# Optimization experiments

Hardware: AMD Instinct MI355X
Metric: run time of the kernel (lower is better)

## Reference

```python
import jax, jax.numpy as jnp
import numpy as np

K = 7  # g_decode_kernel_size


def _linear(x, W, b):
    # torch nn.Linear: y = x @ W.T + b, W: [out, in]
    return jnp.matmul(x, W.T) + b


def _shifted_conv(x, w, b):
    # x: [B, D, L]; causal conv: pad left K-1 (== pad both sides K-1 then trim right K-1)
    y = jax.lax.conv_general_dilated(
        x, w, window_strides=(1,), padding=[(K - 1, 0)],
        dimension_numbers=("NCH", "OIH", "NCH"))
    y = y + b[None, :, None]  # [B, 2D, L]
    D = x.shape[1]
    gated = y[:, :D, :] * jax.nn.sigmoid(y[:, D:, :])
    return gated + x


def setup_inputs() -> dict:
    key = jax.random.key(0)
    ks = jax.random.split(key, 16)
    B, T, L = 64, 64, 32
    E_enc, emb, D, A, V = 1024, 512, 512, 512, 30000

    def rn(k, shape, fan_in):
        return jax.random.normal(k, shape, dtype=jnp.float32) * (1.0 / np.sqrt(fan_in))

    return {
        "features": jax.random.normal(ks[0], (B, T, E_enc), dtype=jnp.float32),
        "captions": jax.random.randint(ks[1], (B, L), 0, V),
        "lengths": jax.random.randint(ks[2], (B,), 0, L),
        "embed_W": jax.random.normal(ks[3], (V, emb), dtype=jnp.float32) * 0.02,
        "W1": rn(ks[4], (D, emb + E_enc), emb + E_enc),
        "b1": jnp.zeros((D,), jnp.float32),
        "conv_w1": rn(ks[5], (2 * D, D, K), D * K),
        "conv_b1": jnp.zeros((2 * D,), jnp.float32),
        "conv_w2": rn(ks[6], (2 * D, D, K), D * K),
        "conv_b2": jnp.zeros((2 * D,), jnp.float32),
        "Wenc": rn(ks[7], (A, E_enc), E_enc),
        "benc": jnp.zeros((A,), jnp.float32),
        "Wdec": rn(ks[8], (A, D), D),
        "bdec": jnp.zeros((A,), jnp.float32),
        "Wp": rn(ks[9], (1, A), A),
        "bp": jnp.zeros((1,), jnp.float32),
        "W2": rn(ks[10], (V, E_enc + D), E_enc + D),
        "b2": jnp.zeros((V,), jnp.float32),
    }


def reference(features, captions, lengths, embed_W, W1, b1, conv_w1, conv_b1,
              conv_w2, conv_b2, Wenc, benc, Wdec, bdec, Wp, bp, W2, b2):
    # features: [B, T, E_enc]; captions: [B, L] int
    embeddings = embed_W[captions]                      # [B, L, emb]
    enc_mean = jnp.mean(features, axis=1, keepdims=True)  # [B, 1, E_enc]
    enc_mean = jnp.broadcast_to(enc_mean, (features.shape[0], embeddings.shape[1], features.shape[2]))
    x = jnp.concatenate([enc_mean, embeddings], axis=2)  # [B, L, E_enc+emb]
    x = _linear(x, W1, b1)                               # [B, L, D]
    x = jnp.transpose(x, (0, 2, 1))                      # [B, D, L]
    x = _shifted_conv(x, conv_w1, conv_b1)
    x = _shifted_conv(x, conv_w2, conv_b2)
    decode = jnp.transpose(x, (0, 2, 1))[:, :-1, :]      # [B, L-1, D]

    # Attention (vectorized over decode steps). NOTE: original code computes
    # tanh but discards it (assigns to misspelled 'featrues'), so NO tanh here.
    f_att = _linear(features, Wenc, benc)                # [B, T, A]
    d_att = _linear(decode, Wdec, bdec)                  # [B, S, A]
    # linear_prob applied to (f_att[:,None,t]+d_att[:,s,None]) -> scalar scores
    scores = (f_att[:, None, :, :] + d_att[:, :, None, :]) @ Wp[0] + bp[0]  # [B, S, T]
    attw = jax.nn.softmax(scores, axis=-1)               # softmax over T
    ctx = jnp.einsum("bst,bte->bse", attw, features)     # [B, S, E_enc]

    out = jnp.concatenate([ctx, decode], axis=2)         # [B, S, E_enc+D]
    logits = _linear(out, W2, b2)                        # [B, S, vocab]
    return logits
```

## Files before the change

kernel.cpp:

```cpp
#include <hip/hip_runtime.h>
#include <hip/hip_bf16.h>
#include <math.h>

#define B 64
#define T 64
#define E_ENC 1024
#define EMB 512
#define D 512
#define L 32
#define S 31
#define A 512
#define V 30000
#define KSZ 7
#define KC (D * KSZ)

typedef __attribute__((ext_vector_type(8))) short bf16x8;
typedef __attribute__((ext_vector_type(4))) float f32x4;

__device__ __forceinline__ unsigned short f2bf(float f) {
  union { float f; unsigned int u; } x; x.f = f;
  unsigned int r = (x.u + 0x7fffu + ((x.u >> 16) & 1u)) >> 16;
  return (unsigned short)r;
}

__device__ __forceinline__ void gload_lds16(const void* g, void* l) {
  __builtin_amdgcn_global_load_lds(
      (const __attribute__((address_space(1))) unsigned int*)g,
      (__attribute__((address_space(3))) unsigned int*)l, 16, 0, 0);
}

__global__ void k_wv(const float* __restrict__ Wenc, const float* __restrict__ Wp,
                     const float* __restrict__ benc, float* __restrict__ wv,
                     float* __restrict__ c0) {
  __shared__ float sp[4][64];
  __shared__ float red[256];
  int el = threadIdx.x & 63, part = threadIdx.x >> 6;
  int e = blockIdx.x * 64 + el;
  float s = 0.f;
  for (int a = part * 128; a < part * 128 + 128; ++a)
    s += Wp[a] * Wenc[(size_t)a * E_ENC + e];
  sp[part][el] = s;
  __syncthreads();
  if (part == 0) wv[e] = sp[0][el] + sp[1][el] + sp[2][el] + sp[3][el];
  if (blockIdx.x == 0) {
    int t = threadIdx.x;
    float v = Wp[t] * benc[t] + Wp[t + 256] * benc[t + 256];
    red[t] = v;
    __syncthreads();
    for (int off = 128; off > 0; off >>= 1) {
      if (t < off) red[t] += red[t + off];
      __syncthreads();
    }
    if (t == 0) c0[0] = red[0];
  }
}

__global__ void k_mean_ctx(const float* __restrict__ features, const float* __restrict__ wv,
                           const float* __restrict__ c0, unsigned short* __restrict__ enc_meanb,
                           unsigned short* __restrict__ ctxb) {
  int b = blockIdx.x, tid = threadIdx.x;
  const float* fb = features + (size_t)b * T * E_ENC;
  __shared__ float s_attw[T];

  float m0 = 0, m1 = 0, m2 = 0, m3 = 0;
  for (int t = 0; t < T; ++t) {
    const float* r = fb + t * E_ENC;
    m0 += r[tid]; m1 += r[tid + 256]; m2 += r[tid + 512]; m3 += r[tid + 768];
  }
  size_t eb = (size_t)b * E_ENC;
  enc_meanb[eb + tid]       = f2bf(m0 * (1.f / 64.f));
  enc_meanb[eb + tid + 256] = f2bf(m1 * (1.f / 64.f));
  enc_meanb[eb + tid + 512] = f2bf(m2 * (1.f / 64.f));
  enc_meanb[eb + tid + 768] = f2bf(m3 * (1.f / 64.f));

  {
    int t = tid >> 2, part = tid & 3;
    const float* r = fb + t * E_ENC + part * 256;
    const float* wp = wv + part * 256;
    float s = 0.f;
    for (int e = 0; e < 256; e += 4) {
      float4 f4 = *(const float4*)(r + e);
      float4 w4 = *(const float4*)(wp + e);
      s += f4.x * w4.x + f4.y * w4.y + f4.z * w4.z + f4.w * w4.w;
    }
    s += __shfl_xor(s, 1);
    s += __shfl_xor(s, 2);
    if (part == 0) s_attw[t] = s + c0[0];
  }
  __syncthreads();
  if (tid < 64) {
    float v = s_attw[tid];
    float mx = v;
    #pragma unroll
    for (int off = 32; off > 0; off >>= 1) mx = fmaxf(mx, __shfl_xor(mx, off));
    float e = expf(v - mx);
    float sm = e;
    #pragma unroll
    for (int off = 32; off > 0; off >>= 1) sm += __shfl_xor(sm, off);
    s_attw[tid] = e / sm;
  }
  __syncthreads();
  float ca = 0, cb = 0, cc = 0, cd = 0;
  for (int t = 0; t < T; ++t) {
    float w = s_attw[t];
    const float* r = fb + t * E_ENC;
    ca += w * r[tid]; cb += w * r[tid + 256]; cc += w * r[tid + 512]; cd += w * r[tid + 768];
  }
  ctxb[eb + tid]       = f2bf(ca);
  ctxb[eb + tid + 256] = f2bf(cb);
  ctxb[eb + tid + 512] = f2bf(cc);
  ctxb[eb + tid + 768] = f2bf(cd);
}

__global__ void k_gather_emb(const float* __restrict__ embed_W,
                             const int* __restrict__ captions,
                             unsigned short* __restrict__ Xe) {
  int g = blockIdx.x, tid = threadIdx.x;
  int cap = captions[g];
  const float* src = embed_W + (size_t)cap * EMB;
  float2 v = *(const float2*)(src + tid * 2);
  unsigned int pk = (unsigned int)f2bf(v.x) | ((unsigned int)f2bf(v.y) << 16);
  *(unsigned int*)(Xe + (size_t)g * EMB + tid * 2) = pk;
}

__global__ void k_cvt_w1(const float* __restrict__ W1, unsigned short* __restrict__ w1b) {
  int d = blockIdx.x, tid = threadIdx.x;
  #pragma unroll
  for (int i = 0; i < 3; ++i) {
    int c = tid * 2 + i * 512;
    float2 v = *(const float2*)(W1 + (size_t)d * (E_ENC + EMB) + c);
    unsigned int pk = (unsigned int)f2bf(v.x) | ((unsigned int)f2bf(v.y) << 16);
    *(unsigned int*)(w1b + (size_t)d * (E_ENC + EMB) + c) = pk;
  }
}

__global__ __launch_bounds__(256) void k_x1f_mfma(
    const unsigned short* __restrict__ enc_meanb,
    const unsigned short* __restrict__ Xe,
    const unsigned short* __restrict__ w1b,
    const float* __restrict__ b1, float* __restrict__ x1) {
  __shared__ __align__(16) unsigned short As[64 * 64];
  __shared__ __align__(16) unsigned short Bs[64 * 64];
  int c0 = blockIdx.x * 64, g0 = blockIdx.y * 64;
  int tid = threadIdx.x, lane = tid & 63, wave = tid >> 6;
  int wr = wave >> 1, wc = wave & 1;
  int rsel = lane & 15, hi = lane >> 4;

  f32x4 acc[2][2];
  #pragma unroll
  for (int m = 0; m < 2; ++m)
    #pragma unroll
    for (int n = 0; n < 2; ++n) acc[m][n] = (f32x4){0.f, 0.f, 0.f, 0.f};

  int r1 = tid >> 3, s1 = tid & 7;
  int sw = (s1 ^ (r1 & 7)) * 8;
  const unsigned short* emA1 = enc_meanb + (size_t)(g0 >> 5) * 1024 + sw;
  const unsigned short* emA2 = enc_meanb + (size_t)((g0 >> 5) + 1) * 1024 + sw;
  const unsigned short* xeA1 = Xe + (size_t)(g0 + r1) * 512 + sw;
  const unsigned short* xeA2 = Xe + (size_t)(g0 + r1 + 32) * 512 + sw;
  const unsigned short* gB1 = w1b + (size_t)(c0 + r1) * (E_ENC + EMB) + sw;
  const unsigned short* gB2 = w1b + (size_t)(c0 + r1 + 32) * (E_ENC + EMB) + sw;
  unsigned short* aD1 = As + wave * 512;
  unsigned short* aD2 = As + 2048 + wave * 512;
  unsigned short* bD1 = Bs + wave * 512;
  unsigned short* bD2 = Bs + 2048 + wave * 512;

  int slot0 = hi ^ (rsel & 7);
  int slot1 = (4 + hi) ^ (rsel & 7);

  for (int kt = 0; kt < 24; ++kt) {
    const unsigned short *pA1, *pA2;
    if (kt < 16) { pA1 = emA1 + kt * 64; pA2 = emA2 + kt * 64; }
    else         { pA1 = xeA1 + (kt - 16) * 64; pA2 = xeA2 + (kt - 16) * 64; }
    gload_lds16(pA1, aD1);
    gload_lds16(pA2, aD2);
    gload_lds16(gB1, bD1);
    gload_lds16(gB2, bD2);
    gB1 += 64; gB2 += 64;
    __syncthreads();

    bf16x8 af[2][2], bfr[2][2];
    #pragma unroll
    for (int m = 0; m < 2; ++m) {
      int rowA = (wr * 32 + m * 16 + rsel) * 64;
      af[m][0] = *(const bf16x8*)(As + rowA + slot0 * 8);
      af[m][1] = *(const bf16x8*)(As + rowA + slot1 * 8);
    }
    #pragma unroll
    for (int n = 0; n < 2; ++n) {
      int rowB = (wc * 32 + n * 16 + rsel) * 64;
      bfr[n][0] = *(const bf16x8*)(Bs + rowB + slot0 * 8);
      bfr[n][1] = *(const bf16x8*)(Bs + rowB + slot1 * 8);
    }
    #pragma unroll
    for (int m = 0; m < 2; ++m)
      #pragma unroll
      for (int n = 0; n < 2; ++n) {
        acc[m][n] = __builtin_amdgcn_mfma_f32_16x16x32_bf16(af[m][0], bfr[n][0], acc[m][n], 0, 0, 0);
        acc[m][n] = __builtin_amdgcn_mfma_f32_16x16x32_bf16(af[m][1], bfr[n][1], acc[m][n], 0, 0, 0);
      }
    __syncthreads();
  }

  float bvv[2];
  #pragma unroll
  for (int n = 0; n < 2; ++n) bvv[n] = b1[c0 + wc * 32 + n * 16 + rsel];
  #pragma unroll
  for (int m = 0; m < 2; ++m)
    #pragma unroll
    for (int i = 0; i < 4; ++i) {
      int g = g0 + wr * 32 + m * 16 + hi * 4 + i;
      float* xr = x1 + (size_t)g * D;
      #pragma unroll
      for (int n = 0; n < 2; ++n) {
        int c = c0 + wc * 32 + n * 16 + rsel;
        xr[c] = acc[m][n][i] + bvv[n];
      }
    }
}

__global__ void k_im2col(const float* __restrict__ x, unsigned short* __restrict__ Xc) {
  int g = blockIdx.x, tid = threadIdx.x;
  int b = g >> 5, l = g & 31;
  unsigned short* row = Xc + (size_t)g * KC;
  const float* xb = x + (size_t)b * L * D;
  int d = tid * 2;
  #pragma unroll
  for (int k = 0; k < KSZ; ++k) {
    int lp = l + k - 6;
    unsigned int pk = 0;
    if (lp >= 0) {
      float2 v = *(const float2*)(xb + (size_t)lp * D + d);
      pk = (unsigned int)f2bf(v.x) | ((unsigned int)f2bf(v.y) << 16);
    }
    *(unsigned int*)(row + k * 512 + d) = pk;
  }
}

__global__ void k_cvt_wconv(const float* __restrict__ w, unsigned short* __restrict__ wb) {
  __shared__ float row[KC];
  int c = blockIdx.x, tid = threadIdx.x;
  const float* wr = w + (size_t)c * KC;
  for (int i = tid; i < KC; i += 256) row[i] = wr[i];
  __syncthreads();
  unsigned short* ob = wb + (size_t)c * KC;
  int dp = tid * 2;
  #pragma unroll
  for (int k = 0; k < KSZ; ++k) {
    unsigned int pk = (unsigned int)f2bf(row[dp * 7 + k]) |
                      ((unsigned int)f2bf(row[(dp + 1) * 7 + k]) << 16);
    *(unsigned int*)(ob + k * 512 + dp) = pk;
  }
}

template <int OUT_BF16>
__global__ __launch_bounds__(256) void k_conv_glu(
    const unsigned short* __restrict__ Xc, const unsigned short* __restrict__ wb,
    const float* __restrict__ bias, const float* __restrict__ xres,
    float* __restrict__ outf, unsigned short* __restrict__ outh) {
  __shared__ __align__(16) unsigned char csmem[32768];
  unsigned short (*As)[64 * 64] = (unsigned short (*)[64 * 64])csmem;
  unsigned short (*Bs)[64 * 64] = (unsigned short (*)[64 * 64])(csmem + 16384);
  int c0 = blockIdx.x * 32, g0 = blockIdx.y * 64;
  int tid = threadIdx.x, lane = tid & 63, wave = tid >> 6;
  int wr = wave >> 1, wc = wave & 1;
  int rsel = lane & 15, hi = lane >> 4;

  f32x4 acc[2][2];
  #pragma unroll
  for (int m = 0; m < 2; ++m)
    #pragma unroll
    for (int n = 0; n < 2; ++n) acc[m][n] = (f32x4){0.f, 0.f, 0.f, 0.f};

  int r1 = tid >> 3, s1 = tid & 7;
  int sw = (s1 ^ (r1 & 7)) * 8;
  const unsigned short* gA1 = Xc + (size_t)(g0 + r1) * KC + sw;
  const unsigned short* gA2 = Xc + (size_t)(g0 + r1 + 32) * KC + sw;
  const unsigned short* gB1 = wb + (size_t)(c0 + r1) * KC + sw;
  const unsigned short* gB2 = wb + (size_t)(512 + c0 + r1) * KC + sw;

  int slot0 = hi ^ (rsel & 7);
  int slot1 = (4 + hi) ^ (rsel & 7);

  gload_lds16(gA1, &As[0][wave * 512]);
  gload_lds16(gA2, &As[0][2048 + wave * 512]);
  gload_lds16(gB1, &Bs[0][wave * 512]);
  gload_lds16(gB2, &Bs[0][2048 + wave * 512]);
  gA1 += 64; gA2 += 64; gB1 += 64; gB2 += 64;
  __syncthreads();

  int cur = 0;
  for (int kt = 0; kt < KC / 64; ++kt) {
    if (kt + 1 < KC / 64) {
      int nb = cur ^ 1;
      gload_lds16(gA1, &As[nb][wave * 512]);
      gload_lds16(gA2, &As[nb][2048 + wave * 512]);
      gload_lds16(gB1, &Bs[nb][wave * 512]);
      gload_lds16(gB2, &Bs[nb][2048 + wave * 512]);
      gA1 += 64; gA2 += 64; gB1 += 64; gB2 += 64;
    }

    bf16x8 af[2][2], bfr[2][2];
    #pragma unroll
    for (int m = 0; m < 2; ++m) {
      int rowA = (wr * 32 + m * 16 + rsel) * 64;
      af[m][0] = *(const bf16x8*)(&As[cur][rowA + slot0 * 8]);
      af[m][1] = *(const bf16x8*)(&As[cur][rowA + slot1 * 8]);
    }
    #pragma unroll
    for (int n = 0; n < 2; ++n) {
      int rowB = (wc * 32 + n * 16 + rsel) * 64;
      bfr[n][0] = *(const bf16x8*)(&Bs[cur][rowB + slot0 * 8]);
      bfr[n][1] = *(const bf16x8*)(&Bs[cur][rowB + slot1 * 8]);
    }
    #pragma unroll
    for (int m = 0; m < 2; ++m)
      #pragma unroll
      for (int n = 0; n < 2; ++n) {
        acc[m][n] = __builtin_amdgcn_mfma_f32_16x16x32_bf16(af[m][0], bfr[n][0], acc[m][n], 0, 0, 0);
        acc[m][n] = __builtin_amdgcn_mfma_f32_16x16x32_bf16(af[m][1], bfr[n][1], acc[m][n], 0, 0, 0);
      }
    __syncthreads();
    cur ^= 1;
  }

  float* sb = (float*)csmem;
  float bvv[2];
  #pragma unroll
  for (int n = 0; n < 2; ++n)
    bvv[n] = wc ? bias[512 + c0 + n * 16 + rsel] : bias[c0 + n * 16 + rsel];
  if (wc) {
    #pragma unroll
    for (int m = 0; m < 2; ++m)
      #pragma unroll
      for (int i = 0; i < 4; ++i) {
        int lr = wr * 32 + m * 16 + hi * 4 + i;
        #pragma unroll
        for (int n = 0; n < 2; ++n)
          sb[lr * 33 + n * 16 + rsel] = acc[m][n][i] + bvv[n];
      }
  }
  __syncthreads();
  if (!wc) {
    #pragma unroll
    for (int m = 0; m < 2; ++m)
      #pragma unroll
      for (int i = 0; i < 4; ++i) {
        int lr = wr * 32 + m * 16 + hi * 4 + i;
        int g = g0 + lr;
        const float* xr = xres + (size_t)g * 512 + c0;
        #pragma unroll
        for (int n = 0; n < 2; ++n) {
          int d = n * 16 + rsel;
          float ya = acc[m][n][i] + bvv[n];
          float yb = sb[lr * 33 + d];
          float val = ya / (1.f + expf(-yb)) + xr[d];
          if (OUT_BF16) outh[(size_t)g * 512 + c0 + d] = f2bf(val);
          else          outf[(size_t)g * 512 + c0 + d] = val;
        }
      }
  }
}

__global__ __launch_bounds__(256) void k_cbase_mfma(
    const unsigned short* __restrict__ ctxb,
    const float* __restrict__ W2,
    const float* __restrict__ b2, float* __restrict__ cbase) {
  __shared__ __align__(16) unsigned short As[64 * 64];
  __shared__ __align__(16) unsigned short Bs[128 * 64];
  int v0 = blockIdx.x * 128;
  int tid = threadIdx.x, lane = tid & 63, wave = tid >> 6;
  int rsel = lane & 15, hi = lane >> 4;
  int wc = wave;

  f32x4 acc[4][2];
  #pragma unroll
  for (int m = 0; m < 4; ++m)
    #pragma unroll
    for (int n = 0; n < 2; ++n) acc[m][n] = (f32x4){0.f, 0.f, 0.f, 0.f};

  int ra1 = tid >> 3, sa = tid & 7;
  int ra2 = ra1 + 32;
  const unsigned short* gA1 = ctxb + (size_t)ra1 * 1024 + (sa ^ (ra1 & 7)) * 8;
  const unsigned short* gA2 = ctxb + (size_t)ra2 * 1024 + (sa ^ (ra2 & 7)) * 8;
  unsigned short* aD1 = As + wave * 512;
  unsigned short* aD2 = As + 2048 + wave * 512;

  const float* gB[4];
  int bofs[4];
  #pragma unroll
  for (int p = 0; p < 4; ++p) {
    int row = p * 32 + (tid >> 3);
    int seg = tid & 7;
    int vr = v0 + row; if (vr > V - 1) vr = V - 1;
    gB[p] = W2 + (size_t)vr * (E_ENC + D) + seg * 8;
    bofs[p] = row * 64 + (seg ^ (row & 7)) * 8;
  }

  for (int kt = 0; kt < 16; ++kt) {
    gload_lds16(gA1, aD1);
    gload_lds16(gA2, aD2);
    gA1 += 64; gA2 += 64;
    #pragma unroll
    for (int p = 0; p < 4; ++p) {
      float4 f0 = *(const float4*)(gB[p]);
      float4 f1 = *(const float4*)(gB[p] + 4);
      gB[p] += 64;
      bf16x8 o;
      o[0] = (short)f2bf(f0.x); o[1] = (short)f2bf(f0.y);
      o[2] = (short)f2bf(f0.z); o[3] = (short)f2bf(f0.w);
      o[4] = (short)f2bf(f1.x); o[5] = (short)f2bf(f1.y);
      o[6] = (short)f2bf(f1.z); o[7] = (short)f2bf(f1.w);
      *(bf16x8*)(Bs + bofs[p]) = o;
    }
    __syncthreads();

    bf16x8 af[4][2], bfr[2][2];
    #pragma unroll
    for (int m = 0; m < 4; ++m) {
      int rowA = (m * 16 + rsel) * 64;
      #pragma unroll
      for (int kk = 0; kk < 2; ++kk)
        af[m][kk] = *(const bf16x8*)(As + rowA + ((kk * 4 + hi) ^ (rsel & 7)) * 8);
    }
    #pragma unroll
    for (int n = 0; n < 2; ++n) {
      int rowB = (wc * 32 + n * 16 + rsel) * 64;
      #pragma unroll
      for (int kk = 0; kk < 2; ++kk)
        bfr[n][kk] = *(const bf16x8*)(Bs + rowB + ((kk * 4 + hi) ^ (rsel & 7)) * 8);
    }
    #pragma unroll
    for (int kk = 0; kk < 2; ++kk)
      #pragma unroll
      for (int m = 0; m < 4; ++m)
        #pragma unroll
        for (int n = 0; n < 2; ++n)
          acc[m][n] = __builtin_amdgcn_mfma_f32_16x16x32_bf16(af[m][kk], bfr[n][kk], acc[m][n], 0, 0, 0);
    __syncthreads();
  }

  #pragma unroll
  for (int n = 0; n < 2; ++n) {
    int v = v0 + wc * 32 + n * 16 + rsel;
    if (v >= V) continue;
    float bias = b2[v];
    #pragma unroll
    for (int m = 0; m < 4; ++m)
      #pragma unroll
      for (int i = 0; i < 4; ++i) {
        int b = m * 16 + hi * 4 + i;
        cbase[(size_t)b * V + v] = acc[m][n][i] + bias;
      }
  }
}

__global__ void k_cvt_w2d(const float* __restrict__ W2, unsigned short* __restrict__ y) {
  int i = blockIdx.x * 256 + threadIdx.x;
  int row = i >> 7, c = (i & 127) << 2;
  float4 f = *(const float4*)(W2 + (size_t)row * (E_ENC + D) + E_ENC + c);
  ushort4 o;
  o.x = f2bf(f.x); o.y = f2bf(f.y); o.z = f2bf(f.z); o.w = f2bf(f.w);
  *(ushort4*)(y + (size_t)row * D + c) = o;
}

__global__ __launch_bounds__(256) void k_logits_mfma(
    const unsigned short* __restrict__ Ab,
    const unsigned short* __restrict__ Bb,
    const float* __restrict__ cbase, float* __restrict__ out) {
  __shared__ __align__(16) unsigned char smem[49152];
  int flat = blockIdx.x;
  int ord = (flat & 7) * 470 + (flat >> 3);
  int v0 = (ord >> 4) * 128, g0 = (ord & 15) * 128;
  int tid = threadIdx.x, lane = tid & 63, wave = tid >> 6;
  int wr = wave >> 1, wc = wave & 1;
  int rsel = lane & 15, hi = lane >> 4;

  f32x4 acc[4][4];
  #pragma unroll
  for (int m = 0; m < 4; ++m)
    #pragma unroll
    for (int n = 0; n < 4; ++n) acc[m][n] = (f32x4){0.f, 0.f, 0.f, 0.f};

  int r1 = tid >> 2, s1 = tid & 3;
  int seg = (s1 ^ ((r1 >> 1) & 3)) * 8;
  const unsigned short* gA1 = Ab + (size_t)(g0 + r1) * 512 + seg;
  const unsigned short* gA2 = Ab + (size_t)(g0 + r1 + 64) * 512 + seg;
  int vr1 = v0 + r1;      if (vr1 > V - 1) vr1 = V - 1;
  int vr2 = v0 + r1 + 64; if (vr2 > V - 1) vr2 = V - 1;
  const unsigned short* gB1 = Bb + (size_t)vr1 * 512 + seg;
  const unsigned short* gB2 = Bb + (size_t)vr2 * 512 + seg;

  int wofs = wave * 512;

#define L_STAGE(bi)                                                        \
  do {                                                                     \
    unsigned short* aB = (unsigned short*)(smem + (bi) * 8192);            \
    unsigned short* bB = (unsigned short*)(smem + 24576 + (bi) * 8192);    \
    gload_lds16(gA1, aB + wofs);                                           \
    gload_lds16(gA2, aB + 2048 + wofs);                                    \
    gload_lds16(gB1, bB + wofs);                                           \
    gload_lds16(gB2, bB + 2048 + wofs);                                    \
    gA1 += 32; gA2 += 32; gB1 += 32; gB2 += 32;                            \
  } while (0)

  L_STAGE(0);
  L_STAGE(1);

  int sl = (rsel >> 1) & 3;
  int sidx = 2, cidx = 0;
  for (int kt = 0; kt < 16; ++kt) {
    if (kt < 14) L_STAGE(sidx);
    __builtin_amdgcn_sched_barrier(0);
    if (kt < 14)       asm volatile("s_waitcnt vmcnt(8)" ::: "memory");
    else if (kt == 14) asm volatile("s_waitcnt vmcnt(4)" ::: "memory");
    else               asm volatile("s_waitcnt vmcnt(0)" ::: "memory");
    __builtin_amdgcn_sched_barrier(0);
    __builtin_amdgcn_s_barrier();
    __builtin_amdgcn_sched_barrier(0);

    const unsigned short* Ac = (const unsigned short*)(smem + cidx * 8192);
    const unsigned short* Bc = (const unsigned short*)(smem + 24576 + cidx * 8192);
    bf16x8 af[4], bfr[4];
    #pragma unroll
    for (int m = 0; m < 4; ++m)
      af[m] = *(const bf16x8*)(Ac + (wr * 64 + m * 16 + rsel) * 32 + ((hi ^ sl) * 8));
    #pragma unroll
    for (int n = 0; n < 4; ++n)
      bfr[n] = *(const bf16x8*)(Bc + (wc * 64 + n * 16 + rsel) * 32 + ((hi ^ sl) * 8));
    #pragma unroll
    for (int m = 0; m < 4; ++m)
      #pragma unroll
      for (int n = 0; n < 4; ++n)
        acc[m][n] = __builtin_amdgcn_mfma_f32_16x16x32_bf16(af[m], bfr[n], acc[m][n], 0, 0, 0);

    __builtin_amdgcn_sched_barrier(0);
    __builtin_amdgcn_s_barrier();
    sidx = cidx;
    cidx = (cidx + 1 == 3) ? 0 : cidx + 1;
  }
#undef L_STAGE

  float* ebuf = (float*)smem;
  #pragma unroll
  for (int h = 0; h < 2; ++h) {
    if (h) __syncthreads();
    if (wr == h) {
      #pragma unroll
      for (int m = 0; m < 4; ++m)
        #pragma unroll
        for (int i = 0; i < 4; ++i) {
          int lr = m * 16 + hi * 4 + i;
          #pragma unroll
          for (int n = 0; n < 4; ++n)
            ebuf[lr * 132 + wc * 64 + n * 16 + rsel] = acc[m][n][i];
        }
    }
    __syncthreads();
    #pragma unroll
    for (int j = 0; j < 8; ++j) {
      int f = tid + j * 256;
      int lr = f >> 5, c4 = (f & 31) * 4;
      int g = g0 + h * 64 + lr;
      int b = g >> 5, lt = g & 31;
      int v = v0 + c4;
      if (lt < S && v < V) {
        float4 val = *(const float4*)(ebuf + lr * 132 + c4);
        float4 cb4 = *(const float4*)(cbase + (size_t)b * V + v);
        float4 o;
        o.x = val.x + cb4.x; o.y = val.y + cb4.y;
        o.z = val.z + cb4.z; o.w = val.w + cb4.w;
        *(float4*)(out + ((size_t)b * S + lt) * V + v) = o;
      }
    }
  }
}

extern "C" void kernel_launch(void* const* d_in, const int* in_sizes, int n_in,
                              void* d_out, int out_size, void* d_ws, size_t ws_size,
                              hipStream_t stream) {
  const float* features = (const float*)d_in[0];
  const int*   captions = (const int*)d_in[1];
  const float* embed_W  = (const float*)d_in[3];
  const float* W1   = (const float*)d_in[4];
  const float* b1   = (const float*)d_in[5];
  const float* cw1  = (const float*)d_in[6];
  const float* cb1  = (const float*)d_in[7];
  const float* cw2  = (const float*)d_in[8];
  const float* cb2  = (const float*)d_in[9];
  const float* Wenc = (const float*)d_in[10];
  const float* benc = (const float*)d_in[11];
  const float* Wp   = (const float*)d_in[14];
  const float* W2   = (const float*)d_in[16];
  const float* b2   = (const float*)d_in[17];
  float* out = (float*)d_out;

  float* ws = (float*)d_ws;
  float* wv       = ws;
  float* c0       = ws + 1024;
  unsigned short* enc_meanb = (unsigned short*)(ws + 1040);
  unsigned short* ctxb = (unsigned short*)(ws + 66576);
  float* xA       = ws + 164880;
  float* xB       = ws + 1213456;
  float* cbase    = ws + 2262032;
  unsigned short* x3b  = (unsigned short*)xA;
  unsigned short* Xc   = (unsigned short*)(ws + 4359184);
  unsigned short* wbuf = (unsigned short*)(ws + 8029200);
  unsigned short* W2d  = (unsigned short*)(ws + 9864208);
  unsigned short* Xe  = Xc;
  unsigned short* w1b = Xc + 1048576;

  hipLaunchKernelGGL(k_cvt_w2d,  dim3(15000),   dim3(256), 0, stream, W2, W2d);
  hipLaunchKernelGGL(k_wv,       dim3(16),      dim3(256), 0, stream, Wenc, Wp, benc, wv, c0);
  hipLaunchKernelGGL(k_mean_ctx, dim3(B),       dim3(256), 0, stream, features, wv, c0, enc_meanb, ctxb);

  hipLaunchKernelGGL(k_gather_emb, dim3(2048),  dim3(256), 0, stream, embed_W, captions, Xe);
  hipLaunchKernelGGL(k_cvt_w1,     dim3(512),   dim3(256), 0, stream, W1, w1b);
  hipLaunchKernelGGL(k_x1f_mfma,   dim3(8, 32), dim3(256), 0, stream, enc_meanb, Xe, w1b, b1, xA);

  hipLaunchKernelGGL(k_cvt_wconv,   dim3(1024),   dim3(256), 0, stream, cw1, wbuf);
  hipLaunchKernelGGL(k_im2col,      dim3(2048),   dim3(256), 0, stream, xA, Xc);
  hipLaunchKernelGGL(k_conv_glu<0>, dim3(16, 32), dim3(256), 0, stream, Xc, wbuf, cb1, xA, xB, (unsigned short*)nullptr);

  hipLaunchKernelGGL(k_cvt_wconv,   dim3(1024),   dim3(256), 0, stream, cw2, wbuf);
  hipLaunchKernelGGL(k_im2col,      dim3(2048),   dim3(256), 0, stream, xB, Xc);
  hipLaunchKernelGGL(k_conv_glu<1>, dim3(16, 32), dim3(256), 0, stream, Xc, wbuf, cb2, xB, (float*)nullptr, x3b);

  hipLaunchKernelGGL(k_cbase_mfma, dim3(235),   dim3(256), 0, stream, ctxb, W2, b2, cbase);
  hipLaunchKernelGGL(k_logits_mfma, dim3(3760), dim3(256), 0, stream, x3b, W2d, cbase, out);
}
```

Before: 368.3 us.

## Triple-buffer conv GEMM and widen logits K-tile to 64 with double buffering

The conv-GLU GEMM moves from a two-buffer loop with __syncthreads to a three-stage LDS ring. It uses explicit vmcnt waits and raw s_barrier, so two global-to-LDS loads stay in flight while MFMAs run. The logits GEMM goes the other way: it drops from three 32-wide K stages to two 64-wide stages with the XOR swizzle layout used by the conv kernel, halving the number of loop iterations and barriers. Both kernels use more shared memory per block (48KB and 64KB), which can lower occupancy. The logits kernel also gives up one stage of prefetch depth.

```diff
diff --git a/kernel.cpp b/kernel.cpp
--- a/kernel.cpp
+++ b/kernel.cpp
@@ -258,9 +258,7 @@
     const unsigned short* __restrict__ Xc, const unsigned short* __restrict__ wb,
     const float* __restrict__ bias, const float* __restrict__ xres,
     float* __restrict__ outf, unsigned short* __restrict__ outh) {
-  __shared__ __align__(16) unsigned char csmem[32768];
-  unsigned short (*As)[64 * 64] = (unsigned short (*)[64 * 64])csmem;
-  unsigned short (*Bs)[64 * 64] = (unsigned short (*)[64 * 64])(csmem + 16384);
+  __shared__ __align__(16) unsigned char csmem[49152];
   int c0 = blockIdx.x * 32, g0 = blockIdx.y * 64;
   int tid = threadIdx.x, lane = tid & 63, wave = tid >> 6;
   int wr = wave >> 1, wc = wave & 1;
@@ -281,37 +279,47 @@
 
   int slot0 = hi ^ (rsel & 7);
   int slot1 = (4 + hi) ^ (rsel & 7);
-
-  gload_lds16(gA1, &As[0][wave * 512]);
-  gload_lds16(gA2, &As[0][2048 + wave * 512]);
-  gload_lds16(gB1, &Bs[0][wave * 512]);
-  gload_lds16(gB2, &Bs[0][2048 + wave * 512]);
-  gA1 += 64; gA2 += 64; gB1 += 64; gB2 += 64;
-  __syncthreads();
-
-  int cur = 0;
+  int wofs = wave * 512;
+
+#define C_STAGE(bi)                                                        \
+  do {                                                                     \
+    unsigned short* aB = (unsigned short*)(csmem + (bi) * 8192);           \
+    unsigned short* bB = (unsigned short*)(csmem + 24576 + (bi) * 8192);   \
+    gload_lds16(gA1, aB + wofs);                                           \
+    gload_lds16(gA2, aB + 2048 + wofs);                                    \
+    gload_lds16(gB1, bB + wofs);                                           \
+    gload_lds16(gB2, bB + 2048 + wofs);                                    \
+    gA1 += 64; gA2 += 64; gB1 += 64; gB2 += 64;                            \
+  } while (0)
+
+  C_STAGE(0);
+  C_STAGE(1);
+
+  int sidx = 2, cidx = 0;
   for (int kt = 0; kt < KC / 64; ++kt) {
-    if (kt + 1 < KC / 64) {
-      int nb = cur ^ 1;
-      gload_lds16(gA1, &As[nb][wave * 512]);
-      gload_lds16(gA2, &As[nb][2048 + wave * 512]);
-      gload_lds16(gB1, &Bs[nb][wave * 512]);
-      gload_lds16(gB2, &Bs[nb][2048 + wave * 512]);
-      gA1 += 64; gA2 += 64; gB1 += 64; gB2 += 64;
-    }
-
+    if (kt < KC / 64 - 2) C_STAGE(sidx);
+    __builtin_amdgcn_sched_barrier(0);
+    if (kt < KC / 64 - 2)       asm volatile("s_waitcnt vmcnt(8)" ::: "memory");
+    else if (kt == KC / 64 - 2) asm volatile("s_waitcnt vmcnt(4)" ::: "memory");
+    else                        asm volatile("s_waitcnt vmcnt(0)" ::: "memory");
+    __builtin_amdgcn_sched_barrier(0);
+    __builtin_amdgcn_s_barrier();
+    __builtin_amdgcn_sched_barrier(0);
+
+    const unsigned short* Ac = (const unsigned short*)(csmem + cidx * 8192);
+    const unsigned short* Bc = (const unsigned short*)(csmem + 24576 + cidx * 8192);
     bf16x8 af[2][2], bfr[2][2];
     #pragma unroll
     for (int m = 0; m < 2; ++m) {
       int rowA = (wr * 32 + m * 16 + rsel) * 64;
-      af[m][0] = *(const bf16x8*)(&As[cur][rowA + slot0 * 8]);
-      af[m][1] = *(const bf16x8*)(&As[cur][rowA + slot1 * 8]);
+      af[m][0] = *(const bf16x8*)(Ac + rowA + slot0 * 8);
+      af[m][1] = *(const bf16x8*)(Ac + rowA + slot1 * 8);
     }
     #pragma unroll
     for (int n = 0; n < 2; ++n) {
       int rowB = (wc * 32 + n * 16 + rsel) * 64;
-      bfr[n][0] = *(const bf16x8*)(&Bs[cur][rowB + slot0 * 8]);
-      bfr[n][1] = *(const bf16x8*)(&Bs[cur][rowB + slot1 * 8]);
+      bfr[n][0] = *(const bf16x8*)(Bc + rowB + slot0 * 8);
+      bfr[n][1] = *(const bf16x8*)(Bc + rowB + slot1 * 8);
     }
     #pragma unroll
     for (int m = 0; m < 2; ++m)
@@ -320,9 +328,12 @@
         acc[m][n] = __builtin_amdgcn_mfma_f32_16x16x32_bf16(af[m][0], bfr[n][0], acc[m][n], 0, 0, 0);
         acc[m][n] = __builtin_amdgcn_mfma_f32_16x16x32_bf16(af[m][1], bfr[n][1], acc[m][n], 0, 0, 0);
       }
-    __syncthreads();
-    cur ^= 1;
-  }
+    __builtin_amdgcn_sched_barrier(0);
+    __builtin_amdgcn_s_barrier();
+    sidx = cidx;
+    cidx = (cidx + 1 == 3) ? 0 : cidx + 1;
+  }
+#undef C_STAGE
 
   float* sb = (float*)csmem;
   float bvv[2];
@@ -468,7 +479,7 @@
     const unsigned short* __restrict__ Ab,
     const unsigned short* __restrict__ Bb,
     const float* __restrict__ cbase, float* __restrict__ out) {
-  __shared__ __align__(16) unsigned char smem[49152];
+  __shared__ __align__(16) unsigned char smem[65536];
   int flat = blockIdx.x;
   int ord = (flat & 7) * 470 + (flat >> 3);
   int v0 = (ord >> 4) * 128, g0 = (ord & 15) * 128;
@@ -482,62 +493,68 @@
     #pragma unroll
     for (int n = 0; n < 4; ++n) acc[m][n] = (f32x4){0.f, 0.f, 0.f, 0.f};
 
-  int r1 = tid >> 2, s1 = tid & 3;
-  int seg = (s1 ^ ((r1 >> 1) & 3)) * 8;
-  const unsigned short* gA1 = Ab + (size_t)(g0 + r1) * 512 + seg;
-  const unsigned short* gA2 = Ab + (size_t)(g0 + r1 + 64) * 512 + seg;
-  int vr1 = v0 + r1;      if (vr1 > V - 1) vr1 = V - 1;
-  int vr2 = v0 + r1 + 64; if (vr2 > V - 1) vr2 = V - 1;
-  const unsigned short* gB1 = Bb + (size_t)vr1 * 512 + seg;
-  const unsigned short* gB2 = Bb + (size_t)vr2 * 512 + seg;
-
+  int r1 = tid >> 3, s1 = tid & 7;
+  int sw = (s1 ^ (r1 & 7)) * 8;
+  const unsigned short* gA[4];
+  const unsigned short* gB[4];
+  #pragma unroll
+  for (int p = 0; p < 4; ++p) {
+    gA[p] = Ab + (size_t)(g0 + p * 32 + r1) * 512 + sw;
+    int rB = v0 + p * 32 + r1; if (rB > V - 1) rB = V - 1;
+    gB[p] = Bb + (size_t)rB * 512 + sw;
+  }
   int wofs = wave * 512;
 
 #define L_STAGE(bi)                                                        \
   do {                                                                     \
-    unsigned short* aB = (unsigned short*)(smem + (bi) * 8192);            \
-    unsigned short* bB = (unsigned short*)(smem + 24576 + (bi) * 8192);    \
-    gload_lds16(gA1, aB + wofs);                                           \
-    gload_lds16(gA2, aB + 2048 + wofs);                                    \
-    gload_lds16(gB1, bB + wofs);                                           \
-    gload_lds16(gB2, bB + 2048 + wofs);                                    \
-    gA1 += 32; gA2 += 32; gB1 += 32; gB2 += 32;                            \
+    unsigned short* aB = (unsigned short*)(smem + (bi) * 16384);           \
+    unsigned short* bB = (unsigned short*)(smem + 32768 + (bi) * 16384);   \
+    _Pragma("unroll")                                                      \
+    for (int p = 0; p < 4; ++p) {                                          \
+      gload_lds16(gA[p], aB + p * 2048 + wofs);                            \
+      gload_lds16(gB[p], bB + p * 2048 + wofs);                            \
+      gA[p] += 64; gB[p] += 64;                                            \
+    }                                                                      \
   } while (0)
 
   L_STAGE(0);
-  L_STAGE(1);
-
-  int sl = (rsel >> 1) & 3;
-  int sidx = 2, cidx = 0;
-  for (int kt = 0; kt < 16; ++kt) {
-    if (kt < 14) L_STAGE(sidx);
-    __builtin_amdgcn_sched_barrier(0);
-    if (kt < 14)       asm volatile("s_waitcnt vmcnt(8)" ::: "memory");
-    else if (kt == 14) asm volatile("s_waitcnt vmcnt(4)" ::: "memory");
-    else               asm volatile("s_waitcnt vmcnt(0)" ::: "memory");
+
+  int slot0 = hi ^ (rsel & 7);
+  int slot1 = (4 + hi) ^ (rsel & 7);
+  for (int kt = 0; kt < 8; ++kt) {
+    if (kt + 1 < 8) L_STAGE((kt + 1) & 1);
+    __builtin_amdgcn_sched_barrier(0);
+    if (kt < 7) asm volatile("s_waitcnt vmcnt(8)" ::: "memory");
+    else        asm volatile("s_waitcnt vmcnt(0)" ::: "memory");
     __builtin_amdgcn_sched_barrier(0);
     __builtin_amdgcn_s_barrier();
     __builtin_amdgcn_sched_barrier(0);
 
-    const unsigned short* Ac = (const unsigned short*)(smem + cidx * 8192);
-    const unsigned short* Bc = (const unsigned short*)(smem + 24576 + cidx * 8192);
-    bf16x8 af[4], bfr[4];
-    #pragma unroll
-    for (int m = 0; m < 4; ++m)
-      af[m] = *(const bf16x8*)(Ac + (wr * 64 + m * 16 + rsel) * 32 + ((hi ^ sl) * 8));
-    #pragma unroll
-    for (int n = 0; n < 4; ++n)
-      bfr[n] = *(const bf16x8*)(Bc + (wc * 64 + n * 16 + rsel) * 32 + ((hi ^ sl) * 8));
-    #pragma unroll
-    for (int m = 0; m < 4; ++m)
-      #pragma unroll
-      for (int n = 0; n < 4; ++n)
-        acc[m][n] = __builtin_amdgcn_mfma_f32_16x16x32_bf16(af[m], bfr[n], acc[m][n], 0, 0, 0);
+    const unsigned short* Ac = (const unsigned short*)(smem + (kt & 1) * 16384);
+    const unsigned short* Bc = (const unsigned short*)(smem + 32768 + (kt & 1) * 16384);
+    bf16x8 af[4][2], bfr[4][2];
+    #pragma unroll
+    for (int m = 0; m < 4; ++m) {
+      int rowA = (wr * 64 + m * 16 + rsel) * 64;
+      af[m][0] = *(const bf16x8*)(Ac + rowA + slot0 * 8);
+      af[m][1] = *(const bf16x8*)(Ac + rowA + slot1 * 8);
+    }
+    #pragma unroll
+    for (int n = 0; n < 4; ++n) {
+      int rowB = (wc * 64 + n * 16 + rsel) * 64;
+      bfr[n][0] = *(const bf16x8*)(Bc + rowB + slot0 * 8);
+      bfr[n][1] = *(const bf16x8*)(Bc + rowB + slot1 * 8);
+    }
+    #pragma unroll
+    for (int kk = 0; kk < 2; ++kk)
+      #pragma unroll
+      for (int m = 0; m < 4; ++m)
+        #pragma unroll
+        for (int n = 0; n < 4; ++n)
+          acc[m][n] = __builtin_amdgcn_mfma_f32_16x16x32_bf16(af[m][kk], bfr[n][kk], acc[m][n], 0, 0, 0);
 
     __builtin_amdgcn_sched_barrier(0);
     __builtin_amdgcn_s_barrier();
-    sidx = cidx;
-    cidx = (cidx + 1 == 3) ? 0 : cidx + 1;
   }
 #undef L_STAGE
 
```

New measurement: 405.8 us. +10.2%, slower.

## Triple-buffer conv GLU GEMM loads and double-buffer logits GEMM to cut LDS

Applied to the files above, without the earlier changes.

The conv GLU kernel moves from a two-buffer loop with __syncthreads to a three-stage async global-to-LDS pipeline with explicit vmcnt waits and s_barrier, so loads run two tiles ahead. The logits kernel goes the other way, from three LDS stages to two (34816 bytes instead of 49152), issuing the next stage after the compute barrier, to allow more blocks per CU. This trades prefetch depth for occupancy in logits, and more LDS for deeper prefetch in conv. An extra __syncthreads before the logits epilogue keeps it from overwriting stages still in flight.

```diff
diff --git a/kernel.cpp b/kernel.cpp
--- a/kernel.cpp
+++ b/kernel.cpp
@@ -258,9 +258,7 @@
     const unsigned short* __restrict__ Xc, const unsigned short* __restrict__ wb,
     const float* __restrict__ bias, const float* __restrict__ xres,
     float* __restrict__ outf, unsigned short* __restrict__ outh) {
-  __shared__ __align__(16) unsigned char csmem[32768];
-  unsigned short (*As)[64 * 64] = (unsigned short (*)[64 * 64])csmem;
-  unsigned short (*Bs)[64 * 64] = (unsigned short (*)[64 * 64])(csmem + 16384);
+  __shared__ __align__(16) unsigned char csmem[49152];
   int c0 = blockIdx.x * 32, g0 = blockIdx.y * 64;
   int tid = threadIdx.x, lane = tid & 63, wave = tid >> 6;
   int wr = wave >> 1, wc = wave & 1;
@@ -281,37 +279,47 @@
 
   int slot0 = hi ^ (rsel & 7);
   int slot1 = (4 + hi) ^ (rsel & 7);
-
-  gload_lds16(gA1, &As[0][wave * 512]);
-  gload_lds16(gA2, &As[0][2048 + wave * 512]);
-  gload_lds16(gB1, &Bs[0][wave * 512]);
-  gload_lds16(gB2, &Bs[0][2048 + wave * 512]);
-  gA1 += 64; gA2 += 64; gB1 += 64; gB2 += 64;
-  __syncthreads();
-
-  int cur = 0;
+  int wofs = wave * 512;
+
+#define C_STAGE(bi)                                                        \
+  do {                                                                     \
+    unsigned short* aB = (unsigned short*)(csmem + (bi) * 8192);           \
+    unsigned short* bB = (unsigned short*)(csmem + 24576 + (bi) * 8192);   \
+    gload_lds16(gA1, aB + wofs);                                           \
+    gload_lds16(gA2, aB + 2048 + wofs);                                    \
+    gload_lds16(gB1, bB + wofs);                                           \
+    gload_lds16(gB2, bB + 2048 + wofs);                                    \
+    gA1 += 64; gA2 += 64; gB1 += 64; gB2 += 64;                            \
+  } while (0)
+
+  C_STAGE(0);
+  C_STAGE(1);
+
+  int sidx = 2, cidx = 0;
   for (int kt = 0; kt < KC / 64; ++kt) {
-    if (kt + 1 < KC / 64) {
-      int nb = cur ^ 1;
-      gload_lds16(gA1, &As[nb][wave * 512]);
-      gload_lds16(gA2, &As[nb][2048 + wave * 512]);
-      gload_lds16(gB1, &Bs[nb][wave * 512]);
-      gload_lds16(gB2, &Bs[nb][2048 + wave * 512]);
-      gA1 += 64; gA2 += 64; gB1 += 64; gB2 += 64;
-    }
-
+    if (kt < KC / 64 - 2) C_STAGE(sidx);
+    __builtin_amdgcn_sched_barrier(0);
+    if (kt < KC / 64 - 2)       asm volatile("s_waitcnt vmcnt(8)" ::: "memory");
+    else if (kt == KC / 64 - 2) asm volatile("s_waitcnt vmcnt(4)" ::: "memory");
+    else                        asm volatile("s_waitcnt vmcnt(0)" ::: "memory");
+    __builtin_amdgcn_sched_barrier(0);
+    __builtin_amdgcn_s_barrier();
+    __builtin_amdgcn_sched_barrier(0);
+
+    const unsigned short* Ac = (const unsigned short*)(csmem + cidx * 8192);
+    const unsigned short* Bc = (const unsigned short*)(csmem + 24576 + cidx * 8192);
     bf16x8 af[2][2], bfr[2][2];
     #pragma unroll
     for (int m = 0; m < 2; ++m) {
       int rowA = (wr * 32 + m * 16 + rsel) * 64;
-      af[m][0] = *(const bf16x8*)(&As[cur][rowA + slot0 * 8]);
-      af[m][1] = *(const bf16x8*)(&As[cur][rowA + slot1 * 8]);
+      af[m][0] = *(const bf16x8*)(Ac + rowA + slot0 * 8);
+      af[m][1] = *(const bf16x8*)(Ac + rowA + slot1 * 8);
     }
     #pragma unroll
     for (int n = 0; n < 2; ++n) {
       int rowB = (wc * 32 + n * 16 + rsel) * 64;
-      bfr[n][0] = *(const bf16x8*)(&Bs[cur][rowB + slot0 * 8]);
-      bfr[n][1] = *(const bf16x8*)(&Bs[cur][rowB + slot1 * 8]);
+      bfr[n][0] = *(const bf16x8*)(Bc + rowB + slot0 * 8);
+      bfr[n][1] = *(const bf16x8*)(Bc + rowB + slot1 * 8);
     }
     #pragma unroll
     for (int m = 0; m < 2; ++m)
@@ -320,9 +328,12 @@
         acc[m][n] = __builtin_amdgcn_mfma_f32_16x16x32_bf16(af[m][0], bfr[n][0], acc[m][n], 0, 0, 0);
         acc[m][n] = __builtin_amdgcn_mfma_f32_16x16x32_bf16(af[m][1], bfr[n][1], acc[m][n], 0, 0, 0);
       }
-    __syncthreads();
-    cur ^= 1;
-  }
+    __builtin_amdgcn_sched_barrier(0);
+    __builtin_amdgcn_s_barrier();
+    sidx = cidx;
+    cidx = (cidx + 1 == 3) ? 0 : cidx + 1;
+  }
+#undef C_STAGE
 
   float* sb = (float*)csmem;
   float bvv[2];
@@ -468,7 +479,7 @@
     const unsigned short* __restrict__ Ab,
     const unsigned short* __restrict__ Bb,
     const float* __restrict__ cbase, float* __restrict__ out) {
-  __shared__ __align__(16) unsigned char smem[49152];
+  __shared__ __align__(16) unsigned char smem[34816];
   int flat = blockIdx.x;
   int ord = (flat & 7) * 470 + (flat >> 3);
   int v0 = (ord >> 4) * 128, g0 = (ord & 15) * 128;
@@ -496,7 +507,7 @@
 #define L_STAGE(bi)                                                        \
   do {                                                                     \
     unsigned short* aB = (unsigned short*)(smem + (bi) * 8192);            \
-    unsigned short* bB = (unsigned short*)(smem + 24576 + (bi) * 8192);    \
+    unsigned short* bB = (unsigned short*)(smem + 16384 + (bi) * 8192);    \
     gload_lds16(gA1, aB + wofs);                                           \
     gload_lds16(gA2, aB + 2048 + wofs);                                    \
     gload_lds16(gB1, bB + wofs);                                           \
@@ -508,19 +519,16 @@
   L_STAGE(1);
 
   int sl = (rsel >> 1) & 3;
-  int sidx = 2, cidx = 0;
   for (int kt = 0; kt < 16; ++kt) {
-    if (kt < 14) L_STAGE(sidx);
-    __builtin_amdgcn_sched_barrier(0);
-    if (kt < 14)       asm volatile("s_waitcnt vmcnt(8)" ::: "memory");
-    else if (kt == 14) asm volatile("s_waitcnt vmcnt(4)" ::: "memory");
-    else               asm volatile("s_waitcnt vmcnt(0)" ::: "memory");
+    __builtin_amdgcn_sched_barrier(0);
+    if (kt < 15) asm volatile("s_waitcnt vmcnt(4)" ::: "memory");
+    else         asm volatile("s_waitcnt vmcnt(0)" ::: "memory");
     __builtin_amdgcn_sched_barrier(0);
     __builtin_amdgcn_s_barrier();
     __builtin_amdgcn_sched_barrier(0);
 
-    const unsigned short* Ac = (const unsigned short*)(smem + cidx * 8192);
-    const unsigned short* Bc = (const unsigned short*)(smem + 24576 + cidx * 8192);
+    const unsigned short* Ac = (const unsigned short*)(smem + (kt & 1) * 8192);
+    const unsigned short* Bc = (const unsigned short*)(smem + 16384 + (kt & 1) * 8192);
     bf16x8 af[4], bfr[4];
     #pragma unroll
     for (int m = 0; m < 4; ++m)
@@ -536,11 +544,12 @@
 
     __builtin_amdgcn_sched_barrier(0);
     __builtin_amdgcn_s_barrier();
-    sidx = cidx;
-    cidx = (cidx + 1 == 3) ? 0 : cidx + 1;
+    __builtin_amdgcn_sched_barrier(0);
+    if (kt + 2 < 16) L_STAGE(kt & 1);
   }
 #undef L_STAGE
 
+  __syncthreads();
   float* ebuf = (float*)smem;
   #pragma unroll
   for (int h = 0; h < 2; ++h) {
```

Measured after the change: 368.7 us. Within noise of the previous version (+0.1%).
